# Performance work log

Measured on AMD Instinct MI355X. Metric: run time of the kernel, lower is better.

Reference implementation:

```python
import jax, jax.numpy as jnp
import numpy as np

N, D, B, O, E = 4096, 1024, 512, 1, 16  # samples, in_size, bottleneck, out_size, n_tasks
L1_LAMBDA = 1e-4


def setup_inputs() -> dict:
    key = jax.random.key(0)
    ks = jax.random.split(key, 6)
    x = jax.random.normal(ks[0], (N, D), jnp.float32)
    keys = jax.random.randint(ks[1], (N,), 0, E, dtype=jnp.int32)
    W1 = jax.random.normal(ks[2], (E, B, D), jnp.float32) / np.sqrt(D).astype(np.float32)
    b1 = jax.random.normal(ks[3], (E, B), jnp.float32) * 0.01
    W2 = jax.random.normal(ks[4], (E, O, B), jnp.float32) / np.sqrt(B).astype(np.float32)
    b2 = jax.random.normal(ks[5], (E, O), jnp.float32) * 0.01
    return {"x": x, "keys": keys, "W1": W1, "b1": b1, "W2": W2, "b2": b2}


def reference(x, keys, W1, b1, W2, b2):
    """Per-sample task-specific 2-layer bottleneck MLP dispatch.

    x: [N, D] float; keys: [N] int task indices.
    W1: [E, B, D], b1: [E, B], W2: [E, O, B], b2: [E, O].
    Returns (out [N, O], l1_lambda * sum_n L1(params of expert keys[n])).
    """
    n = x.shape[0]
    e = W1.shape[0]
    # Dense MoE dispatch: first linear for all experts, then select per sample.
    h_all = jnp.einsum('nd,ebd->neb', x, W1) + b1[None]          # [N, E, B]
    h = h_all[jnp.arange(n), keys]                                # [N, B]
    h = jax.nn.relu(h)                                            # activation='relu'
    out = jnp.einsum('nb,nob->no', h, W2[keys]) + b2[keys]        # [N, O]
    # L1 of the selected expert's parameters is accumulated once per sample.
    l1_per_expert = (jnp.abs(W1).sum((1, 2)) + jnp.abs(b1).sum(1)
                     + jnp.abs(W2).sum((1, 2)) + jnp.abs(b2).sum(1))  # [E]
    counts = jnp.zeros((e,), x.dtype).at[keys].add(jnp.ones((), x.dtype))
    l1 = jnp.asarray(L1_LAMBDA, x.dtype) * jnp.dot(counts, l1_per_expert)
    return out, l1
```

## Files before the change

kernel.cpp:

```cpp
#include <hip/hip_runtime.h>
#include <hip/hip_bf16.h>

#define N_S 4096
#define D_IN 1024
#define B_BOT 512
#define E_EXP 16
#define L1_LAMBDA 1e-4f

#define MT 64
#define NT 128
#define KC 64
#define PITCH 72
#define MT_GRID 8

typedef float f32x4 __attribute__((ext_vector_type(4)));
typedef short bf16x8 __attribute__((ext_vector_type(8)));


__device__ __forceinline__ ushort4 cvt4(float4 v) {
    union { __hip_bfloat162 b2[2]; ushort4 u4; } u;
    u.b2[0] = __float22bfloat162_rn({v.x, v.y});
    u.b2[1] = __float22bfloat162_rn({v.z, v.w});
    return u.u4;
}

__global__ void sort_kernel(const int* __restrict__ keys, int* counts, int* offs,
                            int* ids) {
    __shared__ int cnt[E_EXP], base[E_EXP], cur[E_EXP];
    const int t = threadIdx.x;
    if (t < E_EXP) cnt[t] = 0;
    __syncthreads();
    int myk[4];
#pragma unroll
    for (int i = 0; i < 4; ++i) {
        myk[i] = keys[i * 1024 + t];
        atomicAdd(&cnt[myk[i]], 1);
    }
    __syncthreads();
    if (t == 0) {
        int s = 0;
        for (int e = 0; e < E_EXP; ++e) { base[e] = s; cur[e] = s; s += cnt[e]; }
    }
    __syncthreads();
    if (t < E_EXP) { counts[t] = cnt[t]; offs[t] = base[t]; }
#pragma unroll
    for (int i = 0; i < 4; ++i) {
        int p = atomicAdd(&cur[myk[i]], 1);
        ids[p] = i * 1024 + t;
    }
}

__global__ void l1_kernel(const float* __restrict__ W1, const float* __restrict__ b1,
                          const float* __restrict__ W2, const float* __restrict__ b2,
                          const int* __restrict__ counts, float* __restrict__ out) {
    const int e = blockIdx.x;
    const int j = blockIdx.y;
    const int t = threadIdx.x;
    const float4* w4 = (const float4*)(W1 + (size_t)e * B_BOT * D_IN + (size_t)j * 65536);
    float s = 0.f;
#pragma unroll 4
    for (int i = 0; i < 64; ++i) {
        float4 v = w4[i * 256 + t];
        s += fabsf(v.x) + fabsf(v.y) + fabsf(v.z) + fabsf(v.w);
    }
    if (j == 0) {
        s += fabsf(b1[e * B_BOT + t]) + fabsf(b1[e * B_BOT + 256 + t]);
        s += fabsf(W2[e * B_BOT + t]) + fabsf(W2[e * B_BOT + 256 + t]);
        if (t == 0) s += fabsf(b2[e]);
    }
#pragma unroll
    for (int off = 32; off > 0; off >>= 1) s += __shfl_down(s, off);
    __shared__ float wsum[4];
    if ((t & 63) == 0) wsum[t >> 6] = s;
    __syncthreads();
    if (t == 0) {
        float tot = wsum[0] + wsum[1] + wsum[2] + wsum[3];
        atomicAdd(&out[N_S], L1_LAMBDA * (float)counts[e] * tot);
    }
}

__global__ __launch_bounds__(256, 2)
void mlp_kernel(const float* __restrict__ x, const float* __restrict__ W1,
                const float* __restrict__ b1, const float* __restrict__ W2,
                const float* __restrict__ b2, const int* __restrict__ counts,
                const int* __restrict__ offs, const int* __restrict__ ids,
                float* __restrict__ out) {
    const int e = blockIdx.x, mt = blockIdx.y, bc = blockIdx.z;
    const int cnt = counts[e];
    const int m0 = mt * MT;
    if (m0 >= cnt) return;
    const int base = offs[e];
    const int t = threadIdx.x;
    const int wave = t >> 6, lane = t & 63;
    const int l15 = lane & 15, qd = lane >> 4;
    const int wm = wave & 1, wn = wave >> 1;

    __shared__ __align__(16) ushort xs[MT * PITCH];
    __shared__ __align__(16) ushort wsh[NT * PITCH];
    __shared__ int sid_s[MT];
    __shared__ float red[2][MT];

    if (t < MT) sid_s[t] = ids[base + min(m0 + t, cnt - 1)];
    __syncthreads();

    float b1v[4], w2v[4];
#pragma unroll
    for (int j = 0; j < 4; ++j) {
        const int colg = bc * NT + 64 * wn + 16 * j + l15;
        b1v[j] = b1[e * B_BOT + colg];
        w2v[j] = W2[e * B_BOT + colg];
    }
    const float b2e = b2[e];

    const float* W1e = W1 + ((size_t)e * B_BOT + (size_t)bc * NT) * D_IN;
    const float* xptr[4]; int xoff[4];
    const float* wptr[8]; int woff[8];
#pragma unroll
    for (int i = 0; i < 4; ++i) {
        const int flat = (i << 8) | t, row = flat >> 4, q = flat & 15;
        xptr[i] = x + (size_t)sid_s[row] * D_IN + q * 4;
        xoff[i] = row * PITCH + q * 4;
    }
#pragma unroll
    for (int i = 0; i < 8; ++i) {
        const int flat = (i << 8) | t, row = flat >> 4, q = flat & 15;
        wptr[i] = W1e + (size_t)row * D_IN + q * 4;
        woff[i] = row * PITCH + q * 4;
    }

    f32x4 acc[2][4];
#pragma unroll
    for (int i = 0; i < 2; ++i)
#pragma unroll
        for (int j = 0; j < 4; ++j) acc[i][j] = (f32x4){0.f, 0.f, 0.f, 0.f};

    float4 xv[4], wv[8];
#pragma unroll
    for (int i = 0; i < 4; ++i) xv[i] = *(const float4*)(xptr[i]);
#pragma unroll
    for (int i = 0; i < 8; ++i) wv[i] = *(const float4*)(wptr[i]);

    for (int c = 0; c < D_IN / KC; ++c) {
        __syncthreads();
#pragma unroll
        for (int i = 0; i < 4; ++i) *(ushort4*)&xs[xoff[i]] = cvt4(xv[i]);
#pragma unroll
        for (int i = 0; i < 8; ++i) *(ushort4*)&wsh[woff[i]] = cvt4(wv[i]);
        __syncthreads();
        if (c < D_IN / KC - 1) {
            const int k = (c + 1) * KC;
#pragma unroll
            for (int i = 0; i < 4; ++i) xv[i] = *(const float4*)(xptr[i] + k);
#pragma unroll
            for (int i = 0; i < 8; ++i) wv[i] = *(const float4*)(wptr[i] + k);
        }
#pragma unroll
        for (int s = 0; s < 2; ++s) {
            const int kk = s * 32 + qd * 8;
            bf16x8 a0 = *(bf16x8*)&xs[(32 * wm + l15) * PITCH + kk];
            bf16x8 a1 = *(bf16x8*)&xs[(32 * wm + 16 + l15) * PITCH + kk];
            bf16x8 bb[4];
#pragma unroll
            for (int j = 0; j < 4; ++j)
                bb[j] = *(bf16x8*)&wsh[(64 * wn + 16 * j + l15) * PITCH + kk];
#pragma unroll
            for (int j = 0; j < 4; ++j) {
                acc[0][j] = __builtin_amdgcn_mfma_f32_16x16x32_bf16(a0, bb[j], acc[0][j], 0, 0, 0);
                acc[1][j] = __builtin_amdgcn_mfma_f32_16x16x32_bf16(a1, bb[j], acc[1][j], 0, 0, 0);
            }
        }
    }

    float p[2][4] = {{0.f, 0.f, 0.f, 0.f}, {0.f, 0.f, 0.f, 0.f}};
#pragma unroll
    for (int j = 0; j < 4; ++j)
#pragma unroll
        for (int i = 0; i < 2; ++i)
#pragma unroll
            for (int r = 0; r < 4; ++r) {
                float h = acc[i][j][r] + b1v[j];
                h = fmaxf(h, 0.f);
                p[i][r] = fmaf(h, w2v[j], p[i][r]);
            }
#pragma unroll
    for (int off = 8; off > 0; off >>= 1)
#pragma unroll
        for (int i = 0; i < 2; ++i)
#pragma unroll
            for (int r = 0; r < 4; ++r) p[i][r] += __shfl_xor(p[i][r], off, 16);
    if (l15 == 0) {
#pragma unroll
        for (int i = 0; i < 2; ++i)
#pragma unroll
            for (int r = 0; r < 4; ++r)
                red[wn][32 * wm + 16 * i + 4 * qd + r] = p[i][r];
    }
    __syncthreads();
    if (t < MT && (m0 + t) < cnt) {
        float v = red[0][t] + red[1][t];
        if (bc == 0) v += b2e;
        atomicAdd(&out[sid_s[t]], v);
    }
}

extern "C" void kernel_launch(void* const* d_in, const int* in_sizes, int n_in,
                              void* d_out, int out_size, void* d_ws, size_t ws_size,
                              hipStream_t stream) {
    const float* x    = (const float*)d_in[0];
    const int*   keys = (const int*)d_in[1];
    const float* W1   = (const float*)d_in[2];
    const float* b1   = (const float*)d_in[3];
    const float* W2   = (const float*)d_in[4];
    const float* b2   = (const float*)d_in[5];
    float* out = (float*)d_out;

    char* ws = (char*)d_ws;
    int* counts = (int*)(ws + 0);
    int* offs   = (int*)(ws + 64);
    int* ids    = (int*)(ws + 128);

    hipMemsetAsync(d_out, 0, (size_t)out_size * sizeof(float), stream);
    sort_kernel<<<1, 1024, 0, stream>>>(keys, counts, offs, ids);
    l1_kernel<<<dim3(E_EXP, 8), 256, 0, stream>>>(W1, b1, W2, b2, counts, out);
    mlp_kernel<<<dim3(E_EXP, MT_GRID, B_BOT / NT), 256, 0, stream>>>(
        x, W1, b1, W2, b2, counts, offs, ids, out);
}
```

Before: 122.5 us.

## Pre-convert W1 and x to bf16 in a fused prep kernel feeding LDS-free MFMA

Replaces the separate sort, L1 and memset steps with one prep kernel. It zeroes the output, builds per-expert sample lists with ballot compaction, and computes L1 partial sums while converting W1 and x to bf16 in the workspace. The MLP kernel then streams bf16 operands straight from global memory into registers with a two-stage software prefetch, dropping the LDS staging and block barriers. It also uses 32-row tiles with 256-column halves and folds the final L1 reduction into one wave. This trades extra conversion writes and rereads, and a fixed per-expert cap of 384 tiled rows, for half-width operand traffic and no in-loop synchronisation.

```diff
diff --git a/kernel.cpp b/kernel.cpp
--- a/kernel.cpp
+++ b/kernel.cpp
@@ -7,11 +7,9 @@
 #define E_EXP 16
 #define L1_LAMBDA 1e-4f
 
-#define MT 64
-#define NT 128
-#define KC 64
-#define PITCH 72
-#define MT_GRID 8
+#define MT 32
+#define MT_GRID 12
+#define IDCAP 512
 
 typedef float f32x4 __attribute__((ext_vector_type(4)));
 typedef short bf16x8 __attribute__((ext_vector_type(8)));
@@ -24,109 +22,126 @@
     return u.u4;
 }
 
-__global__ void sort_kernel(const int* __restrict__ keys, int* counts, int* offs,
-                            int* ids) {
-    __shared__ int cnt[E_EXP], base[E_EXP], cur[E_EXP];
+__global__ __launch_bounds__(256)
+void prep_kernel(const float* __restrict__ x, const int* __restrict__ keys,
+                 const float* __restrict__ W1, const float* __restrict__ b1,
+                 const float* __restrict__ W2, const float* __restrict__ b2,
+                 float* __restrict__ out, int* __restrict__ counts,
+                 float* __restrict__ l1small, float* __restrict__ l1part,
+                 int* __restrict__ ids, ushort* __restrict__ W1b,
+                 ushort* __restrict__ xb) {
+    const int blk = blockIdx.x;
     const int t = threadIdx.x;
-    if (t < E_EXP) cnt[t] = 0;
-    __syncthreads();
-    int myk[4];
-#pragma unroll
-    for (int i = 0; i < 4; ++i) {
-        myk[i] = keys[i * 1024 + t];
-        atomicAdd(&cnt[myk[i]], 1);
-    }
-    __syncthreads();
-    if (t == 0) {
-        int s = 0;
-        for (int e = 0; e < E_EXP; ++e) { base[e] = s; cur[e] = s; s += cnt[e]; }
-    }
-    __syncthreads();
-    if (t < E_EXP) { counts[t] = cnt[t]; offs[t] = base[t]; }
-#pragma unroll
-    for (int i = 0; i < 4; ++i) {
-        int p = atomicAdd(&cur[myk[i]], 1);
-        ids[p] = i * 1024 + t;
-    }
-}
-
-__global__ void l1_kernel(const float* __restrict__ W1, const float* __restrict__ b1,
-                          const float* __restrict__ W2, const float* __restrict__ b2,
-                          const int* __restrict__ counts, float* __restrict__ out) {
-    const int e = blockIdx.x;
-    const int j = blockIdx.y;
-    const int t = threadIdx.x;
-    const float4* w4 = (const float4*)(W1 + (size_t)e * B_BOT * D_IN + (size_t)j * 65536);
-    float s = 0.f;
-#pragma unroll 4
-    for (int i = 0; i < 64; ++i) {
-        float4 v = w4[i * 256 + t];
-        s += fabsf(v.x) + fabsf(v.y) + fabsf(v.z) + fabsf(v.w);
-    }
-    if (j == 0) {
-        s += fabsf(b1[e * B_BOT + t]) + fabsf(b1[e * B_BOT + 256 + t]);
-        s += fabsf(W2[e * B_BOT + t]) + fabsf(W2[e * B_BOT + 256 + t]);
+    if (blk < E_EXP) {
+        const int e = blk;
+        out[e * 256 + t] = 0.f;
+        float s = fabsf(b1[e * B_BOT + t]) + fabsf(b1[e * B_BOT + 256 + t])
+                + fabsf(W2[e * B_BOT + t]) + fabsf(W2[e * B_BOT + 256 + t]);
         if (t == 0) s += fabsf(b2[e]);
-    }
-#pragma unroll
-    for (int off = 32; off > 0; off >>= 1) s += __shfl_down(s, off);
-    __shared__ float wsum[4];
-    if ((t & 63) == 0) wsum[t >> 6] = s;
-    __syncthreads();
-    if (t == 0) {
-        float tot = wsum[0] + wsum[1] + wsum[2] + wsum[3];
-        atomicAdd(&out[N_S], L1_LAMBDA * (float)counts[e] * tot);
+#pragma unroll
+        for (int off = 32; off > 0; off >>= 1) s += __shfl_down(s, off);
+        __shared__ float ws4a[4];
+        __shared__ int cnt_s;
+        if ((t & 63) == 0) ws4a[t >> 6] = s;
+        if (t == 0) cnt_s = 0;
+        __syncthreads();
+        if (t == 0) l1small[e] = ws4a[0] + ws4a[1] + ws4a[2] + ws4a[3];
+        const int lane = t & 63;
+        for (int it = 0; it < N_S / 256; ++it) {
+            const int i = it * 256 + t;
+            const bool m = (keys[i] == e);
+            const unsigned long long mask = __ballot(m);
+            int base = 0;
+            if (lane == 0) base = atomicAdd(&cnt_s, __popcll(mask));
+            base = __shfl(base, 0);
+            if (m) {
+                const int pos = base + __popcll(mask & ((1ull << lane) - 1ull));
+                if (pos < IDCAP) ids[e * IDCAP + pos] = i;
+            }
+        }
+        __syncthreads();
+        if (t == 0) counts[e] = min(cnt_s, IDCAP);
+    } else if (blk < E_EXP + 1024) {
+        const int i = blk - E_EXP;
+        const int e = i >> 6;
+        const long long base = (long long)i * 2048;
+        const float4* __restrict__ src = (const float4*)W1;
+        ushort4* __restrict__ dst = (ushort4*)W1b;
+        float s = 0.f;
+#pragma unroll
+        for (int m = 0; m < 8; ++m) {
+            const long long idx = base + m * 256 + t;
+            float4 v = src[idx];
+            s += fabsf(v.x) + fabsf(v.y) + fabsf(v.z) + fabsf(v.w);
+            dst[idx] = cvt4(v);
+        }
+#pragma unroll
+        for (int off = 32; off > 0; off >>= 1) s += __shfl_down(s, off);
+        __shared__ float ws4b[4];
+        if ((t & 63) == 0) ws4b[t >> 6] = s;
+        __syncthreads();
+        if (t == 0) l1part[i] = ws4b[0] + ws4b[1] + ws4b[2] + ws4b[3];
+    } else {
+        const int i = blk - E_EXP - 1024;
+        const long long base = (long long)i * 2048;
+        const float4* __restrict__ src = (const float4*)x;
+        ushort4* __restrict__ dst = (ushort4*)xb;
+#pragma unroll
+        for (int m = 0; m < 8; ++m) {
+            const long long idx = base + m * 256 + t;
+            dst[idx] = cvt4(src[idx]);
+        }
     }
 }
 
 __global__ __launch_bounds__(256, 2)
-void mlp_kernel(const float* __restrict__ x, const float* __restrict__ W1,
+void mlp_kernel(const ushort* __restrict__ W1b, const ushort* __restrict__ xb,
                 const float* __restrict__ b1, const float* __restrict__ W2,
                 const float* __restrict__ b2, const int* __restrict__ counts,
-                const int* __restrict__ offs, const int* __restrict__ ids,
-                float* __restrict__ out) {
-    const int e = blockIdx.x, mt = blockIdx.y, bc = blockIdx.z;
+                const float* __restrict__ l1small, const float* __restrict__ l1part,
+                const int* __restrict__ ids, float* __restrict__ out) {
+    const int mt = blockIdx.x, nh = blockIdx.y, e = blockIdx.z;
+    const int t = threadIdx.x, wave = t >> 6, lane = t & 63;
+    const int l15 = lane & 15, qd = lane >> 4;
+
+    if (mt == 0 && nh == 0 && e == 0 && wave == 0) {
+        const int el = lane >> 2, sub = lane & 3;
+        float s = 0.f;
+#pragma unroll
+        for (int k = 0; k < 16; ++k) s += l1part[el * 64 + sub * 16 + k];
+        s += __shfl_xor(s, 1);
+        s += __shfl_xor(s, 2);
+        float v = (sub == 0) ? (float)counts[el] * (s + l1small[el]) : 0.f;
+        v += __shfl_xor(v, 4);
+        v += __shfl_xor(v, 8);
+        v += __shfl_xor(v, 16);
+        v += __shfl_xor(v, 32);
+        if (lane == 0) out[N_S] = L1_LAMBDA * v;
+    }
+
     const int cnt = counts[e];
     const int m0 = mt * MT;
     if (m0 >= cnt) return;
-    const int base = offs[e];
-    const int t = threadIdx.x;
-    const int wave = t >> 6, lane = t & 63;
-    const int l15 = lane & 15, qd = lane >> 4;
-    const int wm = wave & 1, wn = wave >> 1;
-
-    __shared__ __align__(16) ushort xs[MT * PITCH];
-    __shared__ __align__(16) ushort wsh[NT * PITCH];
-    __shared__ int sid_s[MT];
-    __shared__ float red[2][MT];
-
-    if (t < MT) sid_s[t] = ids[base + min(m0 + t, cnt - 1)];
-    __syncthreads();
-
+
+    const int colb = nh * 256 + wave * 64;
     float b1v[4], w2v[4];
 #pragma unroll
     for (int j = 0; j < 4; ++j) {
-        const int colg = bc * NT + 64 * wn + 16 * j + l15;
-        b1v[j] = b1[e * B_BOT + colg];
-        w2v[j] = W2[e * B_BOT + colg];
+        const int col = colb + 16 * j + l15;
+        b1v[j] = b1[e * B_BOT + col];
+        w2v[j] = W2[e * B_BOT + col];
     }
     const float b2e = b2[e];
 
-    const float* W1e = W1 + ((size_t)e * B_BOT + (size_t)bc * NT) * D_IN;
-    const float* xptr[4]; int xoff[4];
-    const float* wptr[8]; int woff[8];
-#pragma unroll
-    for (int i = 0; i < 4; ++i) {
-        const int flat = (i << 8) | t, row = flat >> 4, q = flat & 15;
-        xptr[i] = x + (size_t)sid_s[row] * D_IN + q * 4;
-        xoff[i] = row * PITCH + q * 4;
-    }
-#pragma unroll
-    for (int i = 0; i < 8; ++i) {
-        const int flat = (i << 8) | t, row = flat >> 4, q = flat & 15;
-        wptr[i] = W1e + (size_t)row * D_IN + q * 4;
-        woff[i] = row * PITCH + q * 4;
-    }
+    const int idb = e * IDCAP;
+    const int s0 = ids[idb + min(m0 + l15, cnt - 1)];
+    const int s1 = ids[idb + min(m0 + 16 + l15, cnt - 1)];
+    const ushort* ap0 = xb + (size_t)s0 * D_IN + qd * 8;
+    const ushort* ap1 = xb + (size_t)s1 * D_IN + qd * 8;
+    const ushort* bp[4];
+#pragma unroll
+    for (int j = 0; j < 4; ++j)
+        bp[j] = W1b + (size_t)(e * B_BOT + colb + 16 * j + l15) * D_IN + qd * 8;
 
     f32x4 acc[2][4];
 #pragma unroll
@@ -134,41 +149,30 @@
 #pragma unroll
         for (int j = 0; j < 4; ++j) acc[i][j] = (f32x4){0.f, 0.f, 0.f, 0.f};
 
-    float4 xv[4], wv[8];
-#pragma unroll
-    for (int i = 0; i < 4; ++i) xv[i] = *(const float4*)(xptr[i]);
-#pragma unroll
-    for (int i = 0; i < 8; ++i) wv[i] = *(const float4*)(wptr[i]);
-
-    for (int c = 0; c < D_IN / KC; ++c) {
-        __syncthreads();
-#pragma unroll
-        for (int i = 0; i < 4; ++i) *(ushort4*)&xs[xoff[i]] = cvt4(xv[i]);
-#pragma unroll
-        for (int i = 0; i < 8; ++i) *(ushort4*)&wsh[woff[i]] = cvt4(wv[i]);
-        __syncthreads();
-        if (c < D_IN / KC - 1) {
-            const int k = (c + 1) * KC;
-#pragma unroll
-            for (int i = 0; i < 4; ++i) xv[i] = *(const float4*)(xptr[i] + k);
-#pragma unroll
-            for (int i = 0; i < 8; ++i) wv[i] = *(const float4*)(wptr[i] + k);
-        }
-#pragma unroll
-        for (int s = 0; s < 2; ++s) {
-            const int kk = s * 32 + qd * 8;
-            bf16x8 a0 = *(bf16x8*)&xs[(32 * wm + l15) * PITCH + kk];
-            bf16x8 a1 = *(bf16x8*)&xs[(32 * wm + 16 + l15) * PITCH + kk];
-            bf16x8 bb[4];
-#pragma unroll
-            for (int j = 0; j < 4; ++j)
-                bb[j] = *(bf16x8*)&wsh[(64 * wn + 16 * j + l15) * PITCH + kk];
-#pragma unroll
-            for (int j = 0; j < 4; ++j) {
-                acc[0][j] = __builtin_amdgcn_mfma_f32_16x16x32_bf16(a0, bb[j], acc[0][j], 0, 0, 0);
-                acc[1][j] = __builtin_amdgcn_mfma_f32_16x16x32_bf16(a1, bb[j], acc[1][j], 0, 0, 0);
-            }
-        }
+    bf16x8 a0c, a1c, bc[4], a0n, a1n, bn[4];
+    a0c = *(const bf16x8*)(ap0);      a1c = *(const bf16x8*)(ap1);
+#pragma unroll
+    for (int j = 0; j < 4; ++j) bc[j] = *(const bf16x8*)(bp[j]);
+    a0n = *(const bf16x8*)(ap0 + 32); a1n = *(const bf16x8*)(ap1 + 32);
+#pragma unroll
+    for (int j = 0; j < 4; ++j) bn[j] = *(const bf16x8*)(bp[j] + 32);
+
+#pragma unroll 2
+    for (int c = 0; c < D_IN / 32; ++c) {
+        const int kp = (c + 2 < D_IN / 32 ? c + 2 : c) * 32;
+        bf16x8 a0t = *(const bf16x8*)(ap0 + kp);
+        bf16x8 a1t = *(const bf16x8*)(ap1 + kp);
+        bf16x8 bt[4];
+#pragma unroll
+        for (int j = 0; j < 4; ++j) bt[j] = *(const bf16x8*)(bp[j] + kp);
+#pragma unroll
+        for (int j = 0; j < 4; ++j) {
+            acc[0][j] = __builtin_amdgcn_mfma_f32_16x16x32_bf16(a0c, bc[j], acc[0][j], 0, 0, 0);
+            acc[1][j] = __builtin_amdgcn_mfma_f32_16x16x32_bf16(a1c, bc[j], acc[1][j], 0, 0, 0);
+        }
+        a0c = a0n; a1c = a1n; a0n = a0t; a1n = a1t;
+#pragma unroll
+        for (int j = 0; j < 4; ++j) { bc[j] = bn[j]; bn[j] = bt[j]; }
     }
 
     float p[2][4] = {{0.f, 0.f, 0.f, 0.f}, {0.f, 0.f, 0.f, 0.f}};
@@ -178,8 +182,7 @@
         for (int i = 0; i < 2; ++i)
 #pragma unroll
             for (int r = 0; r < 4; ++r) {
-                float h = acc[i][j][r] + b1v[j];
-                h = fmaxf(h, 0.f);
+                const float h = fmaxf(acc[i][j][r] + b1v[j], 0.f);
                 p[i][r] = fmaf(h, w2v[j], p[i][r]);
             }
 #pragma unroll
@@ -188,18 +191,22 @@
         for (int i = 0; i < 2; ++i)
 #pragma unroll
             for (int r = 0; r < 4; ++r) p[i][r] += __shfl_xor(p[i][r], off, 16);
+
+    __shared__ float red[4][32];
     if (l15 == 0) {
 #pragma unroll
         for (int i = 0; i < 2; ++i)
 #pragma unroll
-            for (int r = 0; r < 4; ++r)
-                red[wn][32 * wm + 16 * i + 4 * qd + r] = p[i][r];
+            for (int r = 0; r < 4; ++r) red[wave][16 * i + 4 * qd + r] = p[i][r];
     }
     __syncthreads();
-    if (t < MT && (m0 + t) < cnt) {
-        float v = red[0][t] + red[1][t];
-        if (bc == 0) v += b2e;
-        atomicAdd(&out[sid_s[t]], v);
+    if (t < MT) {
+        const int m = m0 + t;
+        if (m < cnt) {
+            float v = red[0][t] + red[1][t] + red[2][t] + red[3][t];
+            if (nh == 0) v += b2e;
+            atomicAdd(&out[ids[idb + m]], v);
+        }
     }
 }
 
@@ -215,13 +222,15 @@
     float* out = (float*)d_out;
 
     char* ws = (char*)d_ws;
-    int* counts = (int*)(ws + 0);
-    int* offs   = (int*)(ws + 64);
-    int* ids    = (int*)(ws + 128);
-
-    hipMemsetAsync(d_out, 0, (size_t)out_size * sizeof(float), stream);
-    sort_kernel<<<1, 1024, 0, stream>>>(keys, counts, offs, ids);
-    l1_kernel<<<dim3(E_EXP, 8), 256, 0, stream>>>(W1, b1, W2, b2, counts, out);
-    mlp_kernel<<<dim3(E_EXP, MT_GRID, B_BOT / NT), 256, 0, stream>>>(
-        x, W1, b1, W2, b2, counts, offs, ids, out);
-}
+    int*    counts  = (int*)(ws + 0);
+    float*  l1small = (float*)(ws + 64);
+    float*  l1part  = (float*)(ws + 128);
+    int*    ids     = (int*)(ws + 4224);
+    ushort* W1b     = (ushort*)(ws + 65536);
+    ushort* xb      = (ushort*)(ws + 65536 + 16777216);
+
+    prep_kernel<<<E_EXP + 1024 + 512, 256, 0, stream>>>(
+        x, keys, W1, b1, W2, b2, out, counts, l1small, l1part, ids, W1b, xb);
+    mlp_kernel<<<dim3(MT_GRID, 2, E_EXP), 256, 0, stream>>>(
+        W1b, xb, b1, W2, b2, counts, l1small, l1part, ids, out);
+}
```

Result: slower. 145.0 us (+18.3%).
